# Optimization experiments

Hardware: AMD Instinct MI355X
Metric: run time of the kernel (lower is better)

## Reference

```python
import jax, jax.numpy as jnp
import numpy as np

ALPHA = 0.8
TOPK = 9
LOW_BOUND = 0.0
EPS = 1e-10
IOU_EPS = 1e-6


def pairwise_iou(boxes1, boxes2):
    # boxes1 [N,4], boxes2 [G,4] in x1,y1,x2,y2 -> IoU [N,G] (mmdet BboxOverlaps2D)
    area1 = (boxes1[:, 2] - boxes1[:, 0]) * (boxes1[:, 3] - boxes1[:, 1])  # [N]
    area2 = (boxes2[:, 2] - boxes2[:, 0]) * (boxes2[:, 3] - boxes2[:, 1])  # [G]
    lt = jnp.maximum(boxes1[:, None, :2], boxes2[None, :, :2])  # [N,G,2]
    rb = jnp.minimum(boxes1[:, None, 2:], boxes2[None, :, 2:])  # [N,G,2]
    wh = jnp.clip(rb - lt, 0.0)
    inter = wh[..., 0] * wh[..., 1]  # [N,G]
    union = area1[:, None] + area2[None, :] - inter
    return inter / jnp.maximum(union, IOU_EPS)


def setup_inputs() -> dict:
    key = jax.random.key(0)
    k1, k2, k3, k4, k5, k6, k7 = jax.random.split(key, 7)
    N, G, C = 65536, 256, 80
    IMG = 1024.0
    points = jax.random.uniform(k1, (N, 2), dtype=jnp.float32) * IMG  # (cy, cx)
    p_xy1 = jax.random.uniform(k2, (N, 2), dtype=jnp.float32) * (IMG - 96.0)
    p_wh = jax.random.uniform(k3, (N, 2), dtype=jnp.float32) * 95.0 + 1.0
    bbox_preds = jnp.concatenate([p_xy1, p_xy1 + p_wh], axis=1)  # valid x1y1x2y2
    g_xy1 = jax.random.uniform(k4, (G, 2), dtype=jnp.float32) * (IMG - 256.0)
    g_wh = jax.random.uniform(k5, (G, 2), dtype=jnp.float32) * 255.0 + 1.0
    gt_bboxes = jnp.concatenate([g_xy1, g_xy1 + g_wh], axis=1)
    cls_scores = jax.random.normal(k6, (N, C), dtype=jnp.float32)
    gt_labels = jax.random.randint(k7, (G,), 0, C)
    return {"points": points, "cls_scores": cls_scores, "bbox_preds": bbox_preds,
            "gt_bboxes": gt_bboxes, "gt_labels": gt_labels}


def reference(points, cls_scores, bbox_preds, gt_bboxes, gt_labels):
    num_points = points.shape[0]
    num_gt = gt_bboxes.shape[0]
    overlaps = pairwise_iou(bbox_preds, gt_bboxes)  # [N,G]
    cls_cost = jax.nn.sigmoid(cls_scores[:, gt_labels])  # [N,G]
    overlaps = cls_cost ** (1.0 - ALPHA) * overlaps ** ALPHA
    # top-k points per GT (torch: overlaps.topk(k, dim=0))
    _, topk_idxs = jax.lax.top_k(overlaps.T, TOPK)  # [G,K]
    candidate_idxs = topk_idxs.T  # [K,G]
    cp = jnp.transpose(points[candidate_idxs], (1, 0, 2))  # [G,K,2] (cy,cx)
    # mle_2d_gaussian_2: per-GT MLE Gaussian over candidate points
    miu = cp.mean(axis=1, keepdims=True)  # [G,1,2]
    diff = cp - miu  # [G,K,2]
    sigma = jnp.einsum('gki,gkj->gij', diff, diff) / TOPK  # [G,2,2]
    a, b = sigma[:, 0, 0], sigma[:, 0, 1]
    c, d = sigma[:, 1, 0], sigma[:, 1, 1]
    det = a * d - b * c  # [G]
    inv = jnp.stack([jnp.stack([d, -b], axis=-1),
                     jnp.stack([-c, a], axis=-1)], axis=-2) / (det + EPS)[:, None, None]
    maha = jnp.einsum('gki,gij,gkj->gk', diff, inv, diff)  # [G,K]
    candidate_w = jnp.exp(-0.5 * maha).T  # [K,G]
    # center-inside-gt validity, evaluated only at candidate points
    cy, cx = cp[:, :, 0], cp[:, :, 1]  # [G,K]
    gx1, gy1, gx2, gy2 = (gt_bboxes[:, i][:, None] for i in range(4))  # [G,1]
    valid = ((cx - gx1 > EPS) & (cy - gy1 > EPS) &
             (gx2 - cx > EPS) & (gy2 - cy > EPS)).T  # [K,G]
    wv = candidate_w * valid.astype(candidate_w.dtype)
    # scatter per-GT weights to points, then max over GTs == scatter-max
    w = jnp.zeros((num_points,), dtype=cls_scores.dtype)
    w = w.at[candidate_idxs.reshape(-1)].max(wv.reshape(-1))
    w = jnp.where(w < LOW_BOUND, jnp.zeros_like(w), w)
    return w
```

## Files before the change

### kernel.cpp

```cpp
#include <hip/hip_runtime.h>
#include <hip/hip_bf16.h>
#include <math.h>

#define NPTS   65536
#define NGT    256
#define NCLS   80
#define TOPK   9
#define GSLICE 32
#define NPB    256
#define NXB    (NPTS / NPB)
#define SCAP   64

__device__ inline unsigned long long pack_key(float L, unsigned idx) {
    unsigned u   = __float_as_uint(L);
    unsigned k32 = (u & 0x80000000u) ? ~u : (u | 0x80000000u);
    return ((unsigned long long)k32 << 32) | (unsigned)(~idx);
}

__global__ __launch_bounds__(256) void filter_kernel(
    const float* __restrict__ preds,
    const float* __restrict__ gtb,
    unsigned short* __restrict__ counts,
    unsigned long long* __restrict__ bucket,
    float* __restrict__ w)
{
    __shared__ unsigned lcnt[GSLICE];
    __shared__ unsigned long long stage[GSLICE][SCAP];

    const int t   = threadIdx.x;
    const int xb  = blockIdx.x;
    const int g0  = blockIdx.y * GSLICE;
    const int pt  = xb * NPB + t;
    const int bid = blockIdx.y * NXB + xb;

    if (t < GSLICE) lcnt[t] = 0u;
    if (t < 32) w[bid * 32 + t] = 0.0f;

    float4 pb = ((const float4*)preds)[pt];
    float parea = (pb.z - pb.x) * (pb.w - pb.y);
    __syncthreads();

    for (int gi = 0; gi < GSLICE; ++gi) {
        const float4 g4 = ((const float4*)gtb)[g0 + gi];
        float ix1 = fmaxf(pb.x, g4.x), iy1 = fmaxf(pb.y, g4.y);
        float ix2 = fminf(pb.z, g4.z), iy2 = fminf(pb.w, g4.w);
        float iw  = fmaxf(ix2 - ix1, 0.0f);
        float ih  = fmaxf(iy2 - iy1, 0.0f);
        float inter = iw * ih;
        if (inter > 0.0f) {
            float garea = (g4.z - g4.x) * (g4.w - g4.y);
            float uni = fmaxf(parea + garea - inter, 1e-6f);
            float iou = inter / uni;
            unsigned long long entry =
                ((unsigned long long)__float_as_uint(iou) << 32) |
                (unsigned)(~(unsigned)pt);
            unsigned slot = atomicAdd(&lcnt[gi], 1u);
            if (slot < SCAP) stage[gi][slot] = entry;
        }
    }
    __syncthreads();

    if (t < GSLICE) {
        unsigned c = lcnt[t];
        if (c > SCAP) c = SCAP;
        lcnt[t] = c;
        counts[(size_t)(g0 + t) * NXB + xb] = (unsigned short)c;
    }
    __syncthreads();

    for (int i = t; i < GSLICE * SCAP; i += 256) {
        int gi = i >> 6;
        int sl = i & (SCAP - 1);
        if (sl < (int)lcnt[gi])
            bucket[((size_t)(g0 + gi) * NXB + xb) * SCAP + sl] = stage[gi][sl];
    }
}

__global__ __launch_bounds__(256) void select_kernel(
    const unsigned short*     __restrict__ counts,
    const unsigned long long* __restrict__ bucket,
    const float* __restrict__ cls,
    const int*   __restrict__ glab,
    const float* __restrict__ pts,
    const float* __restrict__ gtb,
    float* __restrict__ w)
{
    const int g    = blockIdx.x;
    const int t    = threadIdx.x;
    const int lane = t & 63;
    const int wid  = t >> 6;

    __shared__ unsigned long long wl[4][TOPK];
    __shared__ unsigned tidx[TOPK];
    __shared__ float ppy[TOPK], ppx[TOPK];

    const int lab = glab[g];
    const float E1 = 1.0f - 0.8f;

    unsigned long long loc[TOPK];
#pragma unroll
    for (int k = 0; k < TOPK; ++k) loc[k] = 0ULL;
    if (t < TOPK) loc[0] = pack_key(-INFINITY, (unsigned)t);

    int c = (int)counts[(size_t)g * NXB + t];
    const unsigned long long* src = bucket + ((size_t)g * NXB + t) * SCAP;
    for (int j = 0; j < c; ++j) {
        unsigned long long v = src[j];
        unsigned p = ~(unsigned)(v & 0xFFFFFFFFu);
        float x   = cls[(size_t)p * NCLS + lab];
        float iou = __uint_as_float((unsigned)(v >> 32));
        float s   = 1.0f / (1.0f + expf(-x));
        float L   = E1 * log2f(s) + 0.8f * log2f(iou);
        unsigned u   = __float_as_uint(L);
        unsigned k32 = (u & 0x80000000u) ? ~u : (u | 0x80000000u);
        unsigned long long key =
            ((unsigned long long)k32 << 32) | (v & 0xFFFFFFFFu);
        if (key > loc[TOPK - 1]) {
            loc[TOPK - 1] = key;
#pragma unroll
            for (int jj = TOPK - 1; jj > 0; --jj)
                if (loc[jj] > loc[jj - 1]) {
                    unsigned long long tmp = loc[jj];
                    loc[jj] = loc[jj - 1]; loc[jj - 1] = tmp;
                }
        }
    }
#pragma unroll
    for (int a = 0; a < TOPK; ++a)
#pragma unroll
        for (int j = TOPK - 1; j > 0; --j)
            if (loc[j] > loc[j - 1]) {
                unsigned long long tmp = loc[j];
                loc[j] = loc[j - 1]; loc[j - 1] = tmp;
            }

#pragma unroll
    for (int lvl = 0; lvl < 6; ++lvl) {
        const int off = 1 << lvl;
        unsigned long long oth[TOPK];
#pragma unroll
        for (int k = 0; k < TOPK; ++k) oth[k] = __shfl_xor(loc[k], off);
#pragma unroll
        for (int k = 0; k < TOPK; ++k) {
            unsigned long long v = oth[k];
            if (v > loc[TOPK - 1]) {
                loc[TOPK - 1] = v;
#pragma unroll
                for (int j = TOPK - 1; j > 0; --j) {
                    if (loc[j] > loc[j - 1]) {
                        unsigned long long tmp = loc[j];
                        loc[j] = loc[j - 1]; loc[j - 1] = tmp;
                    }
                }
            }
        }
    }

    if (lane == 0) {
#pragma unroll
        for (int k = 0; k < TOPK; ++k) wl[wid][k] = loc[k];
    }
    __syncthreads();

    if (t == 0) {
#pragma unroll
        for (int wv = 1; wv < 4; ++wv) {
#pragma unroll
            for (int k = 0; k < TOPK; ++k) {
                unsigned long long v = wl[wv][k];
                if (v > loc[TOPK - 1]) {
                    loc[TOPK - 1] = v;
#pragma unroll
                    for (int j = TOPK - 1; j > 0; --j) {
                        if (loc[j] > loc[j - 1]) {
                            unsigned long long tmp = loc[j];
                            loc[j] = loc[j - 1]; loc[j - 1] = tmp;
                        }
                    }
                }
            }
        }
#pragma unroll
        for (int k = 0; k < TOPK; ++k)
            tidx[k] = ~(unsigned)(loc[k] & 0xFFFFFFFFu);
    }
    __syncthreads();

    if (t < TOPK) {
        unsigned pi = tidx[t];
        ppy[t] = pts[2 * (size_t)pi];
        ppx[t] = pts[2 * (size_t)pi + 1];
    }
    __syncthreads();

    if (t == 0) {
        float4 g4 = ((const float4*)gtb)[g];
        float m0 = 0.0f, m1 = 0.0f;
#pragma unroll
        for (int k = 0; k < TOPK; ++k) { m0 += ppy[k]; m1 += ppx[k]; }
        m0 /= (float)TOPK; m1 /= (float)TOPK;

        float d0[TOPK], d1[TOPK];
        float a = 0.0f, bb = 0.0f, dd = 0.0f;
#pragma unroll
        for (int k = 0; k < TOPK; ++k) {
            d0[k] = ppy[k] - m0;
            d1[k] = ppx[k] - m1;
            a  += d0[k] * d0[k];
            bb += d0[k] * d1[k];
            dd += d1[k] * d1[k];
        }
        a /= (float)TOPK; bb /= (float)TOPK; dd /= (float)TOPK;
        float det  = a * dd - bb * bb;
        float rinv = 1.0f / (det + 1e-10f);

#pragma unroll
        for (int k = 0; k < TOPK; ++k) {
            float q = d0[k] * (dd * d0[k] - bb * d1[k])
                    + d1[k] * (a  * d1[k] - bb * d0[k]);
            float maha = q * rinv;
            float wt = expf(-0.5f * maha);
            bool valid = (ppx[k] - g4.x > 1e-10f) && (ppy[k] - g4.y > 1e-10f) &&
                         (g4.z - ppx[k] > 1e-10f) && (g4.w - ppy[k] > 1e-10f);
            float wv = valid ? wt : 0.0f;
            atomicMax((int*)&w[tidx[k]], __float_as_int(wv));
        }
    }
}

extern "C" void kernel_launch(void* const* d_in, const int* in_sizes, int n_in,
                              void* d_out, int out_size, void* d_ws, size_t ws_size,
                              hipStream_t stream) {
    const float* points  = (const float*)d_in[0];
    const float* cls     = (const float*)d_in[1];
    const float* preds   = (const float*)d_in[2];
    const float* gtb     = (const float*)d_in[3];
    const int*   glab    = (const int*)d_in[4];
    float* w = (float*)d_out;

    unsigned long long* bucket = (unsigned long long*)d_ws;
    unsigned short* counts =
        (unsigned short*)((char*)d_ws + (size_t)NGT * NXB * SCAP * 8);

    filter_kernel<<<dim3(NXB, NGT / GSLICE), 256, 0, stream>>>(
        preds, gtb, counts, bucket, w);
    select_kernel<<<NGT, 256, 0, stream>>>(
        counts, bucket, cls, glab, points, gtb, w);
}
```

Measured before the change: 139.7 us.

## Split per-GT top-k selection into parallel scoring and merge kernels

The single per-GT select kernel becomes two kernels. The score kernel launches 8 sub-blocks per GT, and each one scans a fixed slice of bucket slots with coalesced, batched loads and keeps a per-block top-9 using an occupancy mask. A small merge kernel then combines the 8 partial top-9 lists per GT and computes the Gaussian weights and the scatter-max. This replaces the long serial per-thread loop over variable-length buckets, which ran in only 256 blocks, with 8x more blocks and uniform work per thread. In exchange it adds a kernel launch, a partial-results round trip through memory, and reads of bucket slots that are empty and then masked out.

```diff
diff --git a/kernel.cpp b/kernel.cpp
--- a/kernel.cpp
+++ b/kernel.cpp
@@ -10,6 +10,8 @@
 #define NPB    256
 #define NXB    (NPTS / NPB)
 #define SCAP   64
+#define NSUB   8
+#define SEGPB  (NXB / NSUB)
 
 __device__ inline unsigned long long pack_key(float L, unsigned idx) {
     unsigned u   = __float_as_uint(L);
@@ -76,11 +78,134 @@
     }
 }
 
-__global__ __launch_bounds__(256) void select_kernel(
+__global__ __launch_bounds__(256) void score_kernel(
     const unsigned short*     __restrict__ counts,
     const unsigned long long* __restrict__ bucket,
     const float* __restrict__ cls,
     const int*   __restrict__ glab,
+    unsigned long long* __restrict__ partial)
+{
+    const int g    = blockIdx.x;
+    const int sub  = blockIdx.y;
+    const int t    = threadIdx.x;
+    const int lane = t & 63;
+    const int wid  = t >> 6;
+
+    __shared__ unsigned scnt[SEGPB];
+    __shared__ unsigned long long wl[4][TOPK];
+
+    if (t < SEGPB)
+        scnt[t] = counts[(size_t)g * NXB + sub * SEGPB + t];
+    const int lab = glab[g];
+    const float E1 = 1.0f - 0.8f;
+    __syncthreads();
+
+    unsigned long long loc[TOPK];
+#pragma unroll
+    for (int k = 0; k < TOPK; ++k) loc[k] = 0ULL;
+    if (sub == 0 && t < TOPK) loc[0] = pack_key(-INFINITY, (unsigned)t);
+
+    const unsigned long long* base =
+        bucket + ((size_t)g * NXB + (size_t)sub * SEGPB) * SCAP;
+
+    for (int it = 0; it < 8; it += 4) {
+        int idx[4];
+        unsigned long long e[4];
+        float x[4];
+#pragma unroll
+        for (int j = 0; j < 4; ++j) {
+            idx[j] = (it + j) * 256 + t;
+            e[j] = base[idx[j]];
+        }
+#pragma unroll
+        for (int j = 0; j < 4; ++j) {
+            unsigned p = (~(unsigned)(e[j] & 0xFFFFFFFFu)) & 0xFFFFu;
+            x[j] = cls[(size_t)p * NCLS + lab];
+        }
+#pragma unroll
+        for (int j = 0; j < 4; ++j) {
+            bool valid = (unsigned)(idx[j] & (SCAP - 1)) < scnt[idx[j] >> 6];
+            float iou = __uint_as_float((unsigned)(e[j] >> 32));
+            float s   = 1.0f / (1.0f + expf(-x[j]));
+            float L   = E1 * log2f(s) + 0.8f * log2f(iou);
+            unsigned u   = __float_as_uint(L);
+            unsigned k32 = (u & 0x80000000u) ? ~u : (u | 0x80000000u);
+            unsigned long long key =
+                ((unsigned long long)k32 << 32) | (e[j] & 0xFFFFFFFFu);
+            if (valid && key > loc[TOPK - 1]) {
+                loc[TOPK - 1] = key;
+#pragma unroll
+                for (int jj = TOPK - 1; jj > 0; --jj)
+                    if (loc[jj] > loc[jj - 1]) {
+                        unsigned long long tmp = loc[jj];
+                        loc[jj] = loc[jj - 1]; loc[jj - 1] = tmp;
+                    }
+            }
+        }
+    }
+#pragma unroll
+    for (int a = 0; a < TOPK; ++a)
+#pragma unroll
+        for (int j = TOPK - 1; j > 0; --j)
+            if (loc[j] > loc[j - 1]) {
+                unsigned long long tmp = loc[j];
+                loc[j] = loc[j - 1]; loc[j - 1] = tmp;
+            }
+
+#pragma unroll
+    for (int lvl = 0; lvl < 6; ++lvl) {
+        const int off = 1 << lvl;
+        unsigned long long oth[TOPK];
+#pragma unroll
+        for (int k = 0; k < TOPK; ++k) oth[k] = __shfl_xor(loc[k], off);
+#pragma unroll
+        for (int k = 0; k < TOPK; ++k) {
+            unsigned long long v = oth[k];
+            if (v > loc[TOPK - 1]) {
+                loc[TOPK - 1] = v;
+#pragma unroll
+                for (int j = TOPK - 1; j > 0; --j) {
+                    if (loc[j] > loc[j - 1]) {
+                        unsigned long long tmp = loc[j];
+                        loc[j] = loc[j - 1]; loc[j - 1] = tmp;
+                    }
+                }
+            }
+        }
+    }
+
+    if (lane == 0) {
+#pragma unroll
+        for (int k = 0; k < TOPK; ++k) wl[wid][k] = loc[k];
+    }
+    __syncthreads();
+
+    if (t == 0) {
+#pragma unroll
+        for (int wv = 1; wv < 4; ++wv) {
+#pragma unroll
+            for (int k = 0; k < TOPK; ++k) {
+                unsigned long long v = wl[wv][k];
+                if (v > loc[TOPK - 1]) {
+                    loc[TOPK - 1] = v;
+#pragma unroll
+                    for (int j = TOPK - 1; j > 0; --j) {
+                        if (loc[j] > loc[j - 1]) {
+                            unsigned long long tmp = loc[j];
+                            loc[j] = loc[j - 1]; loc[j - 1] = tmp;
+                        }
+                    }
+                }
+            }
+        }
+#pragma unroll
+        for (int k = 0; k < TOPK; ++k)
+            partial[((size_t)g * NSUB + sub) * TOPK + k] = loc[k];
+    }
+}
+
+__global__ __launch_bounds__(128) void merge_kernel(
+    const unsigned long long* __restrict__ partial,
     const float* __restrict__ pts,
     const float* __restrict__ gtb,
     float* __restrict__ w)
@@ -90,49 +215,15 @@
     const int lane = t & 63;
     const int wid  = t >> 6;
 
-    __shared__ unsigned long long wl[4][TOPK];
+    __shared__ unsigned long long wl[2][TOPK];
     __shared__ unsigned tidx[TOPK];
     __shared__ float ppy[TOPK], ppx[TOPK];
 
-    const int lab = glab[g];
-    const float E1 = 1.0f - 0.8f;
-
     unsigned long long loc[TOPK];
 #pragma unroll
     for (int k = 0; k < TOPK; ++k) loc[k] = 0ULL;
-    if (t < TOPK) loc[0] = pack_key(-INFINITY, (unsigned)t);
-
-    int c = (int)counts[(size_t)g * NXB + t];
-    const unsigned long long* src = bucket + ((size_t)g * NXB + t) * SCAP;
-    for (int j = 0; j < c; ++j) {
-        unsigned long long v = src[j];
-        unsigned p = ~(unsigned)(v & 0xFFFFFFFFu);
-        float x   = cls[(size_t)p * NCLS + lab];
-        float iou = __uint_as_float((unsigned)(v >> 32));
-        float s   = 1.0f / (1.0f + expf(-x));
-        float L   = E1 * log2f(s) + 0.8f * log2f(iou);
-        unsigned u   = __float_as_uint(L);
-        unsigned k32 = (u & 0x80000000u) ? ~u : (u | 0x80000000u);
-        unsigned long long key =
-            ((unsigned long long)k32 << 32) | (v & 0xFFFFFFFFu);
-        if (key > loc[TOPK - 1]) {
-            loc[TOPK - 1] = key;
-#pragma unroll
-            for (int jj = TOPK - 1; jj > 0; --jj)
-                if (loc[jj] > loc[jj - 1]) {
-                    unsigned long long tmp = loc[jj];
-                    loc[jj] = loc[jj - 1]; loc[jj - 1] = tmp;
-                }
-        }
-    }
-#pragma unroll
-    for (int a = 0; a < TOPK; ++a)
-#pragma unroll
-        for (int j = TOPK - 1; j > 0; --j)
-            if (loc[j] > loc[j - 1]) {
-                unsigned long long tmp = loc[j];
-                loc[j] = loc[j - 1]; loc[j - 1] = tmp;
-            }
+    if (t < NSUB * TOPK)
+        loc[0] = partial[(size_t)g * (NSUB * TOPK) + t];
 
 #pragma unroll
     for (int lvl = 0; lvl < 6; ++lvl) {
@@ -164,18 +255,15 @@
 
     if (t == 0) {
 #pragma unroll
-        for (int wv = 1; wv < 4; ++wv) {
-#pragma unroll
-            for (int k = 0; k < TOPK; ++k) {
-                unsigned long long v = wl[wv][k];
-                if (v > loc[TOPK - 1]) {
-                    loc[TOPK - 1] = v;
-#pragma unroll
-                    for (int j = TOPK - 1; j > 0; --j) {
-                        if (loc[j] > loc[j - 1]) {
-                            unsigned long long tmp = loc[j];
-                            loc[j] = loc[j - 1]; loc[j - 1] = tmp;
-                        }
+        for (int k = 0; k < TOPK; ++k) {
+            unsigned long long v = wl[1][k];
+            if (v > loc[TOPK - 1]) {
+                loc[TOPK - 1] = v;
+#pragma unroll
+                for (int j = TOPK - 1; j > 0; --j) {
+                    if (loc[j] > loc[j - 1]) {
+                        unsigned long long tmp = loc[j];
+                        loc[j] = loc[j - 1]; loc[j - 1] = tmp;
                     }
                 }
             }
@@ -238,12 +326,16 @@
     const int*   glab    = (const int*)d_in[4];
     float* w = (float*)d_out;
 
-    unsigned long long* bucket = (unsigned long long*)d_ws;
-    unsigned short* counts =
-        (unsigned short*)((char*)d_ws + (size_t)NGT * NXB * SCAP * 8);
+    char* ws = (char*)d_ws;
+    unsigned long long* bucket = (unsigned long long*)ws;
+    size_t off = (size_t)NGT * NXB * SCAP * sizeof(unsigned long long);
+    unsigned short* counts = (unsigned short*)(ws + off);
+    off += (size_t)NGT * NXB * sizeof(unsigned short);
+    unsigned long long* partial = (unsigned long long*)(ws + off);
 
     filter_kernel<<<dim3(NXB, NGT / GSLICE), 256, 0, stream>>>(
         preds, gtb, counts, bucket, w);
-    select_kernel<<<NGT, 256, 0, stream>>>(
-        counts, bucket, cls, glab, points, gtb, w);
-}
+    score_kernel<<<dim3(NGT, NSUB), 256, 0, stream>>>(
+        counts, bucket, cls, glab, partial);
+    merge_kernel<<<NGT, 128, 0, stream>>>(partial, points, gtb, w);
+}
```

Result: slower. 184.8 us (+32.3%).

## Move score computation into filter kernel and widen select kernel to 1024 threads

Applied to the files above, without the earlier changes.

The class-score gather, sigmoid and log-domain score are now computed in the highly parallel filter kernel, which writes final sort keys to the bucket. The select kernel then only reads keys, using 1024 threads per GT with strided, coalesced loads guarded by per-chunk counts staged in shared memory. This is meant to remove the serial, uncoalesced per-thread bucket walk and its scattered class-score loads from the 256-block select kernel. In exchange, the filter kernel does extra gathers, and the select kernel reads whole bucket slots, including empty ones, and has a larger 16-wave final merge.

```diff
diff --git a/kernel.cpp b/kernel.cpp
--- a/kernel.cpp
+++ b/kernel.cpp
@@ -20,11 +20,14 @@
 __global__ __launch_bounds__(256) void filter_kernel(
     const float* __restrict__ preds,
     const float* __restrict__ gtb,
+    const int*   __restrict__ glab,
+    const float* __restrict__ cls,
     unsigned short* __restrict__ counts,
     unsigned long long* __restrict__ bucket,
     float* __restrict__ w)
 {
     __shared__ unsigned lcnt[GSLICE];
+    __shared__ int      glabs[GSLICE];
     __shared__ unsigned long long stage[GSLICE][SCAP];
 
     const int t   = threadIdx.x;
@@ -33,7 +36,10 @@
     const int pt  = xb * NPB + t;
     const int bid = blockIdx.y * NXB + xb;
 
-    if (t < GSLICE) lcnt[t] = 0u;
+    if (t < GSLICE) {
+        lcnt[t]  = 0u;
+        glabs[t] = glab[g0 + t];
+    }
     if (t < 32) w[bid * 32 + t] = 0.0f;
 
     float4 pb = ((const float4*)preds)[pt];
@@ -68,19 +74,47 @@
     }
     __syncthreads();
 
-    for (int i = t; i < GSLICE * SCAP; i += 256) {
-        int gi = i >> 6;
-        int sl = i & (SCAP - 1);
-        if (sl < (int)lcnt[gi])
-            bucket[((size_t)(g0 + gi) * NXB + xb) * SCAP + sl] = stage[gi][sl];
-    }
-}
-
-__global__ __launch_bounds__(256) void select_kernel(
+    const float E1 = 1.0f - 0.8f;
+#pragma unroll
+    for (int k = 0; k < 8; k += 4) {
+        unsigned long long e[4];
+        bool  vld[4];
+        int   gi[4];
+        float x[4];
+#pragma unroll
+        for (int j = 0; j < 4; ++j) {
+            int i = (k + j) * 256 + t;
+            gi[j] = i >> 6;
+            int sl = i & (SCAP - 1);
+            e[j]   = stage[gi[j]][sl];
+            vld[j] = sl < (int)lcnt[gi[j]];
+        }
+#pragma unroll
+        for (int j = 0; j < 4; ++j) {
+            if (vld[j]) {
+                unsigned p = ~(unsigned)(e[j] & 0xFFFFFFFFu);
+                x[j] = cls[(size_t)p * NCLS + glabs[gi[j]]];
+            }
+        }
+#pragma unroll
+        for (int j = 0; j < 4; ++j) {
+            if (vld[j]) {
+                float iou = __uint_as_float((unsigned)(e[j] >> 32));
+                float s   = 1.0f / (1.0f + expf(-x[j]));
+                float L   = E1 * log2f(s) + 0.8f * log2f(iou);
+                unsigned u   = __float_as_uint(L);
+                unsigned k32 = (u & 0x80000000u) ? ~u : (u | 0x80000000u);
+                int i = (k + j) * 256 + t;
+                bucket[((size_t)(g0 + gi[j]) * NXB + xb) * SCAP + (i & (SCAP - 1))]
+                    = ((unsigned long long)k32 << 32) | (e[j] & 0xFFFFFFFFu);
+            }
+        }
+    }
+}
+
+__global__ __launch_bounds__(1024) void select_kernel(
     const unsigned short*     __restrict__ counts,
     const unsigned long long* __restrict__ bucket,
-    const float* __restrict__ cls,
-    const int*   __restrict__ glab,
     const float* __restrict__ pts,
     const float* __restrict__ gtb,
     float* __restrict__ w)
@@ -90,39 +124,42 @@
     const int lane = t & 63;
     const int wid  = t >> 6;
 
-    __shared__ unsigned long long wl[4][TOPK];
+    __shared__ unsigned short scnt[NXB];
+    __shared__ unsigned long long wl[16][TOPK];
     __shared__ unsigned tidx[TOPK];
     __shared__ float ppy[TOPK], ppx[TOPK];
 
-    const int lab = glab[g];
-    const float E1 = 1.0f - 0.8f;
+    if (t < NXB) scnt[t] = counts[(size_t)g * NXB + t];
+    __syncthreads();
 
     unsigned long long loc[TOPK];
 #pragma unroll
     for (int k = 0; k < TOPK; ++k) loc[k] = 0ULL;
     if (t < TOPK) loc[0] = pack_key(-INFINITY, (unsigned)t);
 
-    int c = (int)counts[(size_t)g * NXB + t];
-    const unsigned long long* src = bucket + ((size_t)g * NXB + t) * SCAP;
-    for (int j = 0; j < c; ++j) {
-        unsigned long long v = src[j];
-        unsigned p = ~(unsigned)(v & 0xFFFFFFFFu);
-        float x   = cls[(size_t)p * NCLS + lab];
-        float iou = __uint_as_float((unsigned)(v >> 32));
-        float s   = 1.0f / (1.0f + expf(-x));
-        float L   = E1 * log2f(s) + 0.8f * log2f(iou);
-        unsigned u   = __float_as_uint(L);
-        unsigned k32 = (u & 0x80000000u) ? ~u : (u | 0x80000000u);
-        unsigned long long key =
-            ((unsigned long long)k32 << 32) | (v & 0xFFFFFFFFu);
-        if (key > loc[TOPK - 1]) {
-            loc[TOPK - 1] = key;
-#pragma unroll
-            for (int jj = TOPK - 1; jj > 0; --jj)
-                if (loc[jj] > loc[jj - 1]) {
-                    unsigned long long tmp = loc[jj];
-                    loc[jj] = loc[jj - 1]; loc[jj - 1] = tmp;
-                }
+    const unsigned long long* src = bucket + (size_t)g * (NXB * SCAP);
+
+#pragma unroll
+    for (int k = 0; k < 16; k += 4) {
+        unsigned long long e[4];
+        bool vld[4];
+#pragma unroll
+        for (int j = 0; j < 4; ++j) {
+            int i = (k + j) * 1024 + t;
+            e[j]   = src[i];
+            vld[j] = (i & (SCAP - 1)) < (int)scnt[i >> 6];
+        }
+#pragma unroll
+        for (int j = 0; j < 4; ++j) {
+            if (vld[j] && e[j] > loc[TOPK - 1]) {
+                loc[TOPK - 1] = e[j];
+#pragma unroll
+                for (int jj = TOPK - 1; jj > 0; --jj)
+                    if (loc[jj] > loc[jj - 1]) {
+                        unsigned long long tmp = loc[jj];
+                        loc[jj] = loc[jj - 1]; loc[jj - 1] = tmp;
+                    }
+            }
         }
     }
 #pragma unroll
@@ -164,7 +201,7 @@
 
     if (t == 0) {
 #pragma unroll
-        for (int wv = 1; wv < 4; ++wv) {
+        for (int wv = 1; wv < 16; ++wv) {
 #pragma unroll
             for (int k = 0; k < TOPK; ++k) {
                 unsigned long long v = wl[wv][k];
@@ -238,12 +275,12 @@
     const int*   glab    = (const int*)d_in[4];
     float* w = (float*)d_out;
 
-    unsigned long long* bucket = (unsigned long long*)d_ws;
-    unsigned short* counts =
-        (unsigned short*)((char*)d_ws + (size_t)NGT * NXB * SCAP * 8);
+    char* ws = (char*)d_ws;
+    unsigned long long* bucket = (unsigned long long*)ws;
+    size_t off = (size_t)NGT * NXB * SCAP * sizeof(unsigned long long);
+    unsigned short* counts = (unsigned short*)(ws + off);
 
     filter_kernel<<<dim3(NXB, NGT / GSLICE), 256, 0, stream>>>(
-        preds, gtb, counts, bucket, w);
-    select_kernel<<<NGT, 256, 0, stream>>>(
-        counts, bucket, cls, glab, points, gtb, w);
-}
+        preds, gtb, glab, cls, counts, bucket, w);
+    select_kernel<<<NGT, 1024, 0, stream>>>(counts, bucket, points, gtb, w);
+}
```

Measured after the change: 142.6 us. +2.1%, slower.
